# Kernel tuning notes

Measured on AMD Instinct MI355X. Metric: run time of the kernel, lower is better.

Reference implementation:

```python
import jax, jax.numpy as jnp
import numpy as np

N_RBF = 32
R_CUT = 5.0
LAMBDA = 1.0

# real spherical harmonic constants
_C1 = float(np.sqrt(3.0 / (4.0 * np.pi)))            # l=1
_C2A = float(0.5 * np.sqrt(15.0 / np.pi))            # xy, yz, xz
_C2B = float(0.25 * np.sqrt(5.0 / np.pi))            # 3z^2-1
_C2C = float(0.25 * np.sqrt(15.0 / np.pi))           # x^2-y^2


def _sph_l1_l2(u):
    # u: (P,3) unit vectors -> (P, 3+5) real spherical harmonics for l=1,2
    x, y, z = u[:, 0], u[:, 1], u[:, 2]
    l1 = jnp.stack([_C1 * y, _C1 * z, _C1 * x], axis=-1)
    l2 = jnp.stack([
        _C2A * x * y,
        _C2A * y * z,
        _C2B * (3.0 * z * z - 1.0),
        _C2A * x * z,
        _C2C * (x * x - y * y),
    ], axis=-1)
    return jnp.concatenate([l1, l2], axis=-1)


def setup_inputs() -> dict:
    key = jax.random.key(0)
    k1, k2, k3, k4 = jax.random.split(key, 4)
    n, n_pairs = 100000, 3200000
    R = jax.random.normal(k1, (n, 3), dtype=jnp.float32)
    idx_i = jnp.sort(jax.random.randint(k2, (n_pairs,), 0, n, dtype=jnp.int32))
    idx_j = jax.random.randint(k3, (n_pairs,), 0, n, dtype=jnp.int32)
    z = jax.random.randint(k4, (n,), 0, 100, dtype=jnp.int32)
    pair_mask = jnp.ones((n_pairs,), dtype=jnp.float32)
    point_mask = jnp.ones((n,), dtype=jnp.float32)
    return {"R": R, "pair_mask": pair_mask, "point_mask": point_mask,
            "idx_i": idx_i, "idx_j": idx_j, "z": z}


def reference(R, pair_mask, point_mask, idx_i, idx_j, z):
    # gather + displacement, masked (safe_scale)
    r_ij = (R[idx_j] - R[idx_i]) * pair_mask[:, None]          # (P,3)
    # safe norm (avoid NaN grad at r==0)
    sq = jnp.sum(r_ij * r_ij, axis=-1)
    d_ij = jnp.where(sq == 0, 0.0, jnp.sqrt(jnp.where(sq == 0, 1.0, sq)))
    d_ij = d_ij * pair_mask                                    # (P,)

    # gaussian RBF on equidistant centers in [0, r_cut]
    centers = jnp.linspace(0.0, R_CUT, N_RBF, dtype=jnp.float32)
    width = R_CUT / N_RBF
    rbf_ij = jnp.exp(-0.5 * ((d_ij[:, None] - centers) / width) ** 2)
    rbf_ij = rbf_ij * pair_mask[:, None]                       # (P, n_rbf)

    # cosine cutoff
    phi_r_cut = 0.5 * (jnp.cos(jnp.pi * d_ij / R_CUT) + 1.0)
    phi_r_cut = phi_r_cut * (d_ij < R_CUT).astype(d_ij.dtype) * pair_mask

    # safe unit vector (safe_mask)
    denom = jnp.where(d_ij[:, None] == 0, 1.0, d_ij[:, None])
    unit_r_ij = jnp.where(d_ij[:, None] != 0, r_ij / denom, 0.0)
    unit_r_ij = unit_r_ij * pair_mask[:, None]

    # spherical harmonics for degrees [1,2]
    sph_ij = _sph_l1_l2(unit_r_ij) * pair_mask[:, None]        # (P, 8)

    # SPHC: cutoff-weighted scatter-sum per center atom (bincount over idx_i)
    weighted = sph_ij * phi_r_cut[:, None]                     # (P, 8)
    chi = jax.ops.segment_sum(weighted, idx_i, num_segments=R.shape[0])
    chi = chi * point_mask[:, None] / LAMBDA                   # (n, 8)

    return rbf_ij, chi
```

## Files before the change

### kernel.cpp

```cpp
#include <hip/hip_runtime.h>


#define NRBF 32
constexpr float R_CUT   = 5.0f;
constexpr float WIDTH   = R_CUT / NRBF;
constexpr float INV_W   = 1.0f / WIDTH;
constexpr float CSPACE  = R_CUT / (NRBF - 1);
constexpr float PI_F    = 3.14159265358979323846f;
constexpr float C1  = 0.48860251190291992f;
constexpr float C2A = 1.09254843059207907f;
constexpr float C2B = 0.31539156525252005f;
constexpr float C2C = 0.54627421529603953f;

__global__ __launch_bounds__(256) void geom_pairs_kernel(
    const float* __restrict__ R,
    const float* __restrict__ pair_mask,
    const float* __restrict__ point_mask,
    const int*   __restrict__ idx_i,
    const int*   __restrict__ idx_j,
    float* __restrict__ rbf_out,
    float* __restrict__ chi_out,
    int n_pairs)
{
    const int p    = blockIdx.x * blockDim.x + threadIdx.x;
    const int lane = threadIdx.x & 63;

    int   seg = -1;
    float w[8];
    #pragma unroll
    for (int c = 0; c < 8; ++c) w[c] = 0.0f;

    if (p < n_pairs) {
        const int   i = idx_i[p];
        const int   j = idx_j[p];
        const float m = pair_mask[p];
        seg = i;

        const float rx = (R[3*j+0] - R[3*i+0]) * m;
        const float ry = (R[3*j+1] - R[3*i+1]) * m;
        const float rz = (R[3*j+2] - R[3*i+2]) * m;

        const float sq = rx*rx + ry*ry + rz*rz;
        float d = (sq == 0.0f) ? 0.0f : sqrtf(sq);
        d *= m;

        float rbf[NRBF];
        #pragma unroll
        for (int k = 0; k < NRBF; ++k) {
            const float t = (d - (float)k * CSPACE) * INV_W;
            rbf[k] = __expf(-0.5f * t * t) * m;
        }
        float4* dst = (float4*)(rbf_out + (size_t)p * NRBF);
        #pragma unroll
        for (int k = 0; k < NRBF/4; ++k) {
            dst[k] = make_float4(rbf[4*k+0], rbf[4*k+1], rbf[4*k+2], rbf[4*k+3]);
        }

        float phi = 0.5f * (__cosf(PI_F * d * (1.0f/R_CUT)) + 1.0f);
        phi *= (d < R_CUT) ? 1.0f : 0.0f;
        phi *= m;

        const float inv_d = (d != 0.0f) ? (1.0f / d) : 0.0f;
        const float ux = rx * inv_d * m;
        const float uy = ry * inv_d * m;
        const float uz = rz * inv_d * m;

        float s[8];
        s[0] = C1  * uy;
        s[1] = C1  * uz;
        s[2] = C1  * ux;
        s[3] = C2A * ux * uy;
        s[4] = C2A * uy * uz;
        s[5] = C2B * (3.0f * uz * uz - 1.0f) * m;
        s[6] = C2A * ux * uz;
        s[7] = C2C * (ux * ux - uy * uy);

        const float scale = phi * point_mask[i];
        #pragma unroll
        for (int c = 0; c < 8; ++c) w[c] = s[c] * scale;
    }

    #pragma unroll
    for (int off = 1; off < 64; off <<= 1) {
        const int  oseg = __shfl_down(seg, off, 64);
        const bool ok   = (lane + off < 64) && (oseg == seg);
        #pragma unroll
        for (int c = 0; c < 8; ++c) {
            const float ow = __shfl_down(w[c], off, 64);
            if (ok) w[c] += ow;
        }
    }
    const int  pseg = __shfl_up(seg, 1, 64);
    const bool head = (lane == 0) || (pseg != seg);
    if (head && seg >= 0) {
        float* dst = chi_out + (size_t)seg * 8;
        #pragma unroll
        for (int c = 0; c < 8; ++c) unsafeAtomicAdd(dst + c, w[c]);
    }
}

extern "C" void kernel_launch(void* const* d_in, const int* in_sizes, int n_in,
                              void* d_out, int out_size, void* d_ws, size_t ws_size,
                              hipStream_t stream) {
    const float* R          = (const float*)d_in[0];
    const float* pair_mask  = (const float*)d_in[1];
    const float* point_mask = (const float*)d_in[2];
    const int*   idx_i      = (const int*)d_in[3];
    const int*   idx_j      = (const int*)d_in[4];

    const int n_pairs = in_sizes[1];
    const int n       = in_sizes[2];

    float* rbf_out = (float*)d_out;
    float* chi_out = rbf_out + (size_t)n_pairs * NRBF;

    hipMemsetAsync(chi_out, 0, (size_t)n * 8 * sizeof(float), stream);

    const int block = 256;
    const int grid  = (n_pairs + block - 1) / block;
    geom_pairs_kernel<<<grid, block, 0, stream>>>(
        R, pair_mask, point_mask, idx_i, idx_j, rbf_out, chi_out, n_pairs);
}
```

Before: 564.5 us.

## Coalesce RBF stores via wave shuffles and use exp2 with folded constants

Each thread used to write its own pair's 32 RBF values as eight strided float4 stores. Now the wave shuffles each pair's distance and mask so that 8 lanes cooperatively write one pair's 128-byte row, giving contiguous wave-wide stores. The Gaussian is computed with a native exp2 and a folded constant, which reduces per-element ALU work. This adds shuffle instructions and drops the explicit sq==0 guard, which is harmless here because sqrt(0) is 0.

```diff
diff --git a/kernel.cpp b/kernel.cpp
--- a/kernel.cpp
+++ b/kernel.cpp
@@ -7,6 +7,8 @@
 constexpr float INV_W   = 1.0f / WIDTH;
 constexpr float CSPACE  = R_CUT / (NRBF - 1);
 constexpr float PI_F    = 3.14159265358979323846f;
+constexpr float LOG2E   = 1.44269504088896340736f;
+constexpr float EXP2_A  = -0.5f * LOG2E * INV_W * INV_W;
 constexpr float C1  = 0.48860251190291992f;
 constexpr float C2A = 1.09254843059207907f;
 constexpr float C2B = 0.31539156525252005f;
@@ -26,14 +28,15 @@
     const int lane = threadIdx.x & 63;
 
     int   seg = -1;
+    float d = 0.0f, m = 0.0f;
     float w[8];
     #pragma unroll
     for (int c = 0; c < 8; ++c) w[c] = 0.0f;
 
     if (p < n_pairs) {
-        const int   i = idx_i[p];
-        const int   j = idx_j[p];
-        const float m = pair_mask[p];
+        const int i = idx_i[p];
+        const int j = idx_j[p];
+        m   = pair_mask[p];
         seg = i;
 
         const float rx = (R[3*j+0] - R[3*i+0]) * m;
@@ -41,20 +44,7 @@
         const float rz = (R[3*j+2] - R[3*i+2]) * m;
 
         const float sq = rx*rx + ry*ry + rz*rz;
-        float d = (sq == 0.0f) ? 0.0f : sqrtf(sq);
-        d *= m;
-
-        float rbf[NRBF];
-        #pragma unroll
-        for (int k = 0; k < NRBF; ++k) {
-            const float t = (d - (float)k * CSPACE) * INV_W;
-            rbf[k] = __expf(-0.5f * t * t) * m;
-        }
-        float4* dst = (float4*)(rbf_out + (size_t)p * NRBF);
-        #pragma unroll
-        for (int k = 0; k < NRBF/4; ++k) {
-            dst[k] = make_float4(rbf[4*k+0], rbf[4*k+1], rbf[4*k+2], rbf[4*k+3]);
-        }
+        d = sqrtf(sq) * m;
 
         float phi = 0.5f * (__cosf(PI_F * d * (1.0f/R_CUT)) + 1.0f);
         phi *= (d < R_CUT) ? 1.0f : 0.0f;
@@ -78,6 +68,30 @@
         const float scale = phi * point_mask[i];
         #pragma unroll
         for (int c = 0; c < 8; ++c) w[c] = s[c] * scale;
+    }
+
+    {
+        const long long wbase = (long long)(p - lane);
+        const int sub   = lane & 7;
+        const int grp   = lane >> 3;
+        #pragma unroll
+        for (int it = 0; it < 8; ++it) {
+            const int srcl = it * 8 + grp;
+            const float dd = __shfl(d, srcl, 64);
+            const float mm = __shfl(m, srcl, 64);
+            const long long pr = wbase + srcl;
+            if (pr < (long long)n_pairs) {
+                float v[4];
+                #pragma unroll
+                for (int q = 0; q < 4; ++q) {
+                    const int   k  = 4 * sub + q;
+                    const float dc = dd - (float)k * CSPACE;
+                    v[q] = __builtin_amdgcn_exp2f(EXP2_A * dc * dc) * mm;
+                }
+                float4* dst = (float4*)(rbf_out + pr * NRBF + 4 * sub);
+                *dst = make_float4(v[0], v[1], v[2], v[3]);
+            }
+        }
     }
 
     #pragma unroll
```

Measured after the change: 489.5 us. 1.15x faster.
